# Kernel optimization log

Hardware: AMD Instinct MI355X
Metric: run time of the kernel (lower is better)

The kernel has to match this reference:

```python
import jax, jax.numpy as jnp
import numpy as np

# Rates 40MHz -> 60MHz => Fraction(1.5).limit_denominator(1000) = 3/2
UP, DOWN = 3, 2
MAX_RATE = max(UP, DOWN)
HALF_LEN = 10 * MAX_RATE                      # 30 (scipy.resample_poly default)
N_PRE_PAD = DOWN - (HALF_LEN % DOWN)          # 2
N_PRE_REMOVE = (HALF_LEN + N_PRE_PAD) // DOWN # 16
NUMTAPS_LS = 51
TAIL_ZEROS = 100
B, N = 8, 1048576


def _firwin_kaiser(numtaps, cutoff, beta):
    # scipy.signal.firwin(numtaps, cutoff, window=('kaiser', beta)), cutoff in Nyquist units
    m = np.arange(numtaps) - (numtaps - 1) / 2.0
    h = cutoff * np.sinc(cutoff * m)
    h *= np.kaiser(numtaps, beta)
    return h / h.sum()  # unit DC gain


def _band_int(k, f1, f2):
    # integral_{f1}^{f2} cos(pi*k*f) df, elementwise over integer array k
    k = np.asarray(k, dtype=float)
    safe = np.where(k == 0.0, 1.0, np.pi * k)
    return np.where(k == 0.0, f2 - f1, (np.sin(np.pi * k * f2) - np.sin(np.pi * k * f1)) / safe)


def _firls(numtaps, bands, desired):
    # Type-I linear-phase least-squares FIR (constant desired per band, unit weights)
    M = (numtaps - 1) // 2
    k = np.arange(M + 1)
    Q = np.zeros((M + 1, M + 1))
    rhs = np.zeros(M + 1)
    for f1, f2, d in zip(bands[0::2], bands[1::2], desired[0::2]):
        km = k[:, None] - k[None, :]
        kp = k[:, None] + k[None, :]
        Q += 0.5 * (_band_int(km, f1, f2) + _band_int(kp, f1, f2))
        rhs += d * _band_int(k, f1, f2)
    a = np.linalg.solve(Q, rhs)  # A(f) = sum_n a[n] cos(pi n f)
    half = a / 2.0
    half[0] = a[0]
    return np.concatenate([half[:0:-1], half])  # symmetric impulse response


def setup_inputs() -> dict:
    key = jax.random.key(0)
    x = jax.random.normal(key, (B, N), dtype=jnp.float32)
    # resample_poly anti-imaging filter, scaled by UP, with scipy's zero pre-padding
    h = _firwin_kaiser(2 * HALF_LEN + 1, 1.0 / MAX_RATE, 5.0) * UP
    h = np.concatenate([np.zeros(N_PRE_PAD), h])
    cutoff = DOWN / UP
    b = _firls(NUMTAPS_LS, [0.0, cutoff, cutoff + 0.1, 1.0], [1.0, 1.0, 0.0, 0.0])
    return {
        'x': x,
        'h_resample': jnp.asarray(h, jnp.float32),
        'b_fir': jnp.asarray(b, jnp.float32),
    }


def reference(x, h_resample, b_fir):
    b_sz, n = x.shape
    n_in = b_sz * n
    n_out = n_in * UP // DOWN + (1 if (n_in * UP) % DOWN else 0)
    xf = x.reshape(-1)
    Lh = h_resample.shape[0]
    # Fused polyphase resample: full convolution of UP-zero-stuffed signal
    # with h (flipped for true convolution), decimated by DOWN.
    y = jax.lax.conv_general_dilated(
        xf[None, None, :], h_resample[::-1][None, None, :],
        window_strides=(DOWN,), padding=[(Lh - 1, Lh - 1)],
        lhs_dilation=(UP,),
        dimension_numbers=('NCH', 'OIH', 'NCH'))[0, 0]
    u = y[N_PRE_REMOVE:N_PRE_REMOVE + n_out]               # == scipy.resample_poly
    up_padded = jnp.concatenate([u, jnp.zeros((TAIL_ZEROS,), x.dtype)])
    Lb = b_fir.shape[0]
    # lfilter(b, 1, .) == causal FIR: left-pad Lb-1 zeros, same-length output
    filt = jax.lax.conv_general_dilated(
        up_padded[None, None, :], b_fir[::-1][None, None, :],
        window_strides=(1,), padding=[(Lb - 1, 0)],
        dimension_numbers=('NCH', 'OIH', 'NCH'))[0, 0]
    total = n_out + TAIL_ZEROS
    per_b = total // b_sz
    return filt[:b_sz * per_b].reshape(b_sz, per_b)
```

## Files before the change

### kernel.cpp

```cpp
#include <hip/hip_runtime.h>


#define TPB 256
#define RPT 12
#define OTILE (TPB * RPT)
#define WREG 144
#define NTAPS 55
#define CPSTRIDE 56

#define SLOT(c) ((c) ^ (((c) >> 3) & 7))

__global__ __launch_bounds__(TPB) void prep_k(
    const float* __restrict__ x, const float* __restrict__ h,
    const float* __restrict__ b, float* __restrict__ cp,
    float* __restrict__ out, int n_in, int n_out, int out_size)
{
    __shared__ float h_s[63];
    __shared__ float b_s[51];
    __shared__ float x_s[64];
    __shared__ float u_s[50];

    const int tid = threadIdx.x;
    if (tid < 63) h_s[tid] = h[tid];
    if (tid < 51) b_s[tid] = b[tid];

    if (blockIdx.x == 0) {
        __syncthreads();
        for (int idx = tid; idx < 3 * CPSTRIDE; idx += TPB) {
            const int p = idx / CPSTRIDE;
            const int k = idx - p * CPSTRIDE;
            float acc = 0.0f;
            if (k < NTAPS) {
                const int j = p + 3 * k;
                for (int m = 0; m <= 50; ++m) {
                    const int hi = j - 2 * m;
                    if (hi >= 0 && hi <= 62) acc += b_s[m] * h_s[hi];
                }
            }
            cp[idx] = acc;
        }
    } else if (blockIdx.x == 1) {
        if (tid < 44) x_s[tid] = (tid < n_in) ? x[tid] : 0.0f;
        __syncthreads();
        if (tid < 50) {
            const int s  = 2 * tid + 32;
            const int p0 = s % 3;
            const int q  = s / 3;
            float u = 0.0f;
            #pragma unroll
            for (int i = 0; i <= 20; ++i) {
                const int xi = q - i;
                u += h_s[p0 + 3 * i] * ((xi >= 0) ? x_s[xi] : 0.0f);
            }
            u_s[tid] = u;
        }
        __syncthreads();
        if (tid < 50) {
            float acc = 0.0f;
            for (int t = 0; t <= tid; ++t) acc += b_s[tid - t] * u_s[t];
            out[tid] = acc;
        }
    } else {
        const int t0   = n_out - 50;
        const int qmin = (2 * t0 + 32) / 3;
        const int xb   = qmin - 20;
        if (tid < 64) {
            const int xi = xb + tid;
            x_s[tid] = (xi >= 0 && xi < n_in) ? x[xi] : 0.0f;
        }
        __syncthreads();
        if (tid < 50) {
            const int t  = t0 + tid;
            const int s  = 2 * t + 32;
            const int p0 = s % 3;
            const int q  = s / 3;
            const int base = q - xb;
            float u = 0.0f;
            #pragma unroll
            for (int i = 0; i <= 20; ++i)
                u += h_s[p0 + 3 * i] * x_s[base - i];
            u_s[tid] = u;
        }
        __syncthreads();
        const int n_tail = out_size - n_out;
        if (tid < n_tail) {
            float acc = 0.0f;
            for (int j = tid; j <= 49; ++j) acc += b_s[tid + 50 - j] * u_s[j];
            out[n_out + tid] = acc;
        }
    }
}

__device__ __forceinline__ float co(const int i, const int c0,
                                    const int c1, const int c2) {
    const int ln = i & 63;
    const int v = (i < 64)  ? __builtin_amdgcn_readlane(c0, ln)
                : (i < 128) ? __builtin_amdgcn_readlane(c1, ln)
                            : __builtin_amdgcn_readlane(c2, ln);
    return __int_as_float(v);
}

#define GRP12(g, A, B, C, D) {                                          \
    const float q2x = co(112 + 4*(g), cc0, cc1, cc2);                   \
    const float q2y = co(113 + 4*(g), cc0, cc1, cc2);                   \
    const float q2z = co(114 + 4*(g), cc0, cc1, cc2);                   \
    const float q2w = co(115 + 4*(g), cc0, cc1, cc2);                   \
    const float q1x = co( 56 + 4*(g), cc0, cc1, cc2);                   \
    const float q1y = co( 57 + 4*(g), cc0, cc1, cc2);                   \
    const float q1z = co( 58 + 4*(g), cc0, cc1, cc2);                   \
    const float q1w = co( 59 + 4*(g), cc0, cc1, cc2);                   \
    const float q0x = co(      4*(g), cc0, cc1, cc2);                   \
    const float q0y = co(  1 + 4*(g), cc0, cc1, cc2);                   \
    const float q0z = co(  2 + 4*(g), cc0, cc1, cc2);                   \
    const float q0w = co(  3 + 4*(g), cc0, cc1, cc2);                   \
                                                               \
    a0  += q2x * C.z;  a1  += q1x * C.w;  a2  += q0x * B.x;             \
    a3  += q2x * B.x;  a4  += q1x * B.y;  a5  += q0x * B.z;             \
    a6  += q2x * B.z;  a7  += q1x * B.w;  a8  += q0x * A.x;             \
    a9  += q2x * A.x;  a10 += q1x * A.y;  a11 += q0x * A.z;             \
                                                               \
    a0  += q2y * C.y;  a1  += q1y * C.z;  a2  += q0y * C.w;             \
    a3  += q2y * C.w;  a4  += q1y * B.x;  a5  += q0y * B.y;             \
    a6  += q2y * B.y;  a7  += q1y * B.z;  a8  += q0y * B.w;             \
    a9  += q2y * B.w;  a10 += q1y * A.x;  a11 += q0y * A.y;             \
                                                               \
    a0  += q2z * C.x;  a1  += q1z * C.y;  a2  += q0z * C.z;             \
    a3  += q2z * C.z;  a4  += q1z * C.w;  a5  += q0z * B.x;             \
    a6  += q2z * B.x;  a7  += q1z * B.y;  a8  += q0z * B.z;             \
    a9  += q2z * B.z;  a10 += q1z * B.w;  a11 += q0z * A.x;             \
                                                               \
    a0  += q2w * D.w;  a1  += q1w * C.x;  a2  += q0w * C.y;             \
    a3  += q2w * C.y;  a4  += q1w * C.z;  a5  += q0w * C.w;             \
    a6  += q2w * C.w;  a7  += q1w * B.x;  a8  += q0w * B.y;             \
    a9  += q2w * B.y;  a10 += q1w * B.z;  a11 += q0w * B.w; }

#define GRP12T(g, A, B, C) {                                            \
    const float q2x = co(112 + 4*(g), cc0, cc1, cc2);                   \
    const float q2y = co(113 + 4*(g), cc0, cc1, cc2);                   \
    const float q2z = co(114 + 4*(g), cc0, cc1, cc2);                   \
    const float q1x = co( 56 + 4*(g), cc0, cc1, cc2);                   \
    const float q1y = co( 57 + 4*(g), cc0, cc1, cc2);                   \
    const float q1z = co( 58 + 4*(g), cc0, cc1, cc2);                   \
    const float q0x = co(      4*(g), cc0, cc1, cc2);                   \
    const float q0y = co(  1 + 4*(g), cc0, cc1, cc2);                   \
    const float q0z = co(  2 + 4*(g), cc0, cc1, cc2);                   \
    a0  += q2x * C.z;  a1  += q1x * C.w;  a2  += q0x * B.x;             \
    a3  += q2x * B.x;  a4  += q1x * B.y;  a5  += q0x * B.z;             \
    a6  += q2x * B.z;  a7  += q1x * B.w;  a8  += q0x * A.x;             \
    a9  += q2x * A.x;  a10 += q1x * A.y;  a11 += q0x * A.z;             \
    a0  += q2y * C.y;  a1  += q1y * C.z;  a2  += q0y * C.w;             \
    a3  += q2y * C.w;  a4  += q1y * B.x;  a5  += q0y * B.y;             \
    a6  += q2y * B.y;  a7  += q1y * B.z;  a8  += q0y * B.w;             \
    a9  += q2y * B.w;  a10 += q1y * A.x;  a11 += q0y * A.y;             \
    a0  += q2z * C.x;  a1  += q1z * C.y;  a2  += q0z * C.z;             \
    a3  += q2z * C.z;  a4  += q1z * C.w;  a5  += q0z * B.x;             \
    a6  += q2z * B.x;  a7  += q1z * B.y;  a8  += q0z * B.z;             \
    a9  += q2z * B.z;  a10 += q1z * B.w;  a11 += q0z * A.x; }

__global__ __launch_bounds__(TPB) void fused_fast(
    const float* __restrict__ x, const float* __restrict__ cp,
    float* __restrict__ out, int n_in, int n_out)
{
    __shared__ float4 xs4[4 * WREG];

    const int tid = threadIdx.x;
    const int w   = tid >> 6;
    const int l   = tid & 63;
    const int bt  = blockIdx.x;
    const int o0  = bt * OTILE;
    const int n_tile0 = 2048 * bt - 44;
    const int wreg = w * WREG;

    const int cc0 = __float_as_int(cp[l]);
    const int cc1 = __float_as_int(cp[l + 64]);
    const int cc2 = __float_as_int(cp[(l < 40) ? (128 + l) : 128]);

    const bool interior = (n_tile0 >= 0) && (n_tile0 + 2104 <= n_in);
    if (interior) {
        const float4* gw = (const float4*)(x + n_tile0) + 128 * w;
        const float4 g0 = gw[l];
        const float4 g1 = gw[l + 64];
        xs4[wreg + SLOT(l)]      = g0;
        xs4[wreg + SLOT(l + 64)] = g1;
        if (l < 14) {
            xs4[wreg + SLOT(l + 128)] = gw[l + 128];
        }
    } else {
        const int fb0 = n_tile0 + 512 * w;
        #pragma unroll
        for (int s = 0; s < 3; ++s) {
            const int c = l + 64 * s;
            if (c > 141) break;
            const int fb = fb0 + 4 * c;
            float4 v;
            v.x = (fb + 0 >= 0 && fb + 0 < n_in) ? x[fb + 0] : 0.0f;
            v.y = (fb + 1 >= 0 && fb + 1 < n_in) ? x[fb + 1] : 0.0f;
            v.z = (fb + 2 >= 0 && fb + 2 < n_in) ? x[fb + 2] : 0.0f;
            v.w = (fb + 3 >= 0 && fb + 3 < n_in) ? x[fb + 3] : 0.0f;
            xs4[wreg + SLOT(c)] = v;
        }
    }

    float a0 = 0.f, a1 = 0.f, a2 = 0.f, a3  = 0.f, a4  = 0.f, a5  = 0.f;
    float a6 = 0.f, a7 = 0.f, a8 = 0.f, a9  = 0.f, a10 = 0.f, a11 = 0.f;

#define XS(j) xs4[wreg + SLOT(2 * l + (j))]
    {
        float4 r0 = XS(15), r1 = XS(14), r2 = XS(13),
               r3 = XS(12), r4 = XS(11), r5 = XS(10);
        GRP12( 0, r0, r1, r2, r3);  r0 = XS(9);
        GRP12( 1, r1, r2, r3, r4);  r1 = XS(8);
        GRP12( 2, r2, r3, r4, r5);  r2 = XS(7);
        GRP12( 3, r3, r4, r5, r0);  r3 = XS(6);
        GRP12( 4, r4, r5, r0, r1);  r4 = XS(5);
        GRP12( 5, r5, r0, r1, r2);  r5 = XS(4);
        GRP12( 6, r0, r1, r2, r3);  r0 = XS(3);
        GRP12( 7, r1, r2, r3, r4);  r1 = XS(2);
        GRP12( 8, r2, r3, r4, r5);  r2 = XS(1);
        GRP12( 9, r3, r4, r5, r0);  r3 = XS(0);
        GRP12(10, r4, r5, r0, r1);
        GRP12(11, r5, r0, r1, r2);
        GRP12(12, r0, r1, r2, r3);
        GRP12T(13, r1, r2, r3);
    }
#undef XS

    const int ob = o0 + RPT * tid;
    if (ob >= 50 && ob + 11 < n_out) {
        float4* o4 = (float4*)(out + ob);
        o4[0] = make_float4(a0, a1, a2,  a3);
        o4[1] = make_float4(a4, a5, a6,  a7);
        o4[2] = make_float4(a8, a9, a10, a11);
    } else {
        const float accs[RPT] = {a0, a1, a2, a3, a4, a5, a6, a7, a8, a9, a10, a11};
#pragma unroll
        for (int d = 0; d < RPT; ++d) {
            const int o = ob + d;
            if (o >= 50 && o < n_out) out[o] = accs[d];
        }
    }
}

extern "C" void kernel_launch(void* const* d_in, const int* in_sizes, int n_in_arrs,
                              void* d_out, int out_size, void* d_ws, size_t ws_size,
                              hipStream_t stream) {
    const float* x = (const float*)d_in[0];
    const float* h = (const float*)d_in[1];
    const float* b = (const float*)d_in[2];
    float* out = (float*)d_out;
    float* cp  = (float*)d_ws;

    const int n_in  = in_sizes[0];
    const int n_out = (int)((long long)n_in * 3 / 2);

    prep_k<<<3, TPB, 0, stream>>>(x, h, b, cp, out, n_in, n_out, out_size);

    const int nblocks = (n_out + OTILE - 1) / OTILE;
    fused_fast<<<nblocks, TPB, 0, stream>>>(x, cp, out, n_in, n_out);
}
```

Measured before the change: 106.6 us.

## Process two output tiles per block with both input loads issued upfront

Each block now computes two consecutive output tiles instead of one, so the grid is half as large. Global loads for both tiles' input windows go into registers before the first tile's compute starts, with a sched_barrier keeping the loads grouped. The second tile's load latency is meant to hide behind the first tile's FMA work. The cost is extra live registers for the second tile's staged data and fewer blocks available to hide latency through occupancy.

```diff
diff --git a/kernel.cpp b/kernel.cpp
--- a/kernel.cpp
+++ b/kernel.cpp
@@ -157,6 +157,59 @@
     a6  += q2z * B.x;  a7  += q1z * B.y;  a8  += q0z * B.z;             \
     a9  += q2z * B.z;  a10 += q1z * B.w;  a11 += q0z * A.x; }
 
+#define EDGE_STAGE(NT) {                                                \
+    const int fb0 = (NT) + 512 * w;                                     \
+    _Pragma("unroll")                                                   \
+    for (int s = 0; s < 3; ++s) {                                       \
+        const int c = l + 64 * s;                                       \
+        if (c > 141) break;                                             \
+        const int fb = fb0 + 4 * c;                                     \
+        float4 v;                                                       \
+        v.x = (fb + 0 >= 0 && fb + 0 < n_in) ? x[fb + 0] : 0.0f;        \
+        v.y = (fb + 1 >= 0 && fb + 1 < n_in) ? x[fb + 1] : 0.0f;        \
+        v.z = (fb + 2 >= 0 && fb + 2 < n_in) ? x[fb + 2] : 0.0f;        \
+        v.w = (fb + 3 >= 0 && fb + 3 < n_in) ? x[fb + 3] : 0.0f;        \
+        xs4[wreg + SLOT(c)] = v;                                        \
+    } }
+
+#define XS(j) xs4[wreg + SLOT(2 * l + (j))]
+
+#define TILE_COMPUTE(OB) {                                              \
+    float a0 = 0.f, a1 = 0.f, a2 = 0.f, a3  = 0.f, a4  = 0.f, a5 = 0.f;\
+    float a6 = 0.f, a7 = 0.f, a8 = 0.f, a9  = 0.f, a10 = 0.f, a11 = 0.f;\
+    {                                                                   \
+        float4 r0 = XS(15), r1 = XS(14), r2 = XS(13),                   \
+               r3 = XS(12), r4 = XS(11), r5 = XS(10);                   \
+        GRP12( 0, r0, r1, r2, r3);  r0 = XS(9);                         \
+        GRP12( 1, r1, r2, r3, r4);  r1 = XS(8);                         \
+        GRP12( 2, r2, r3, r4, r5);  r2 = XS(7);                         \
+        GRP12( 3, r3, r4, r5, r0);  r3 = XS(6);                         \
+        GRP12( 4, r4, r5, r0, r1);  r4 = XS(5);                         \
+        GRP12( 5, r5, r0, r1, r2);  r5 = XS(4);                         \
+        GRP12( 6, r0, r1, r2, r3);  r0 = XS(3);                         \
+        GRP12( 7, r1, r2, r3, r4);  r1 = XS(2);                         \
+        GRP12( 8, r2, r3, r4, r5);  r2 = XS(1);                         \
+        GRP12( 9, r3, r4, r5, r0);  r3 = XS(0);                         \
+        GRP12(10, r4, r5, r0, r1);                                      \
+        GRP12(11, r5, r0, r1, r2);                                      \
+        GRP12(12, r0, r1, r2, r3);                                      \
+        GRP12T(13, r1, r2, r3);                                         \
+    }                                                                   \
+    const int ob_ = (OB);                                               \
+    if (ob_ >= 50 && ob_ + 11 < n_out) {                                \
+        float4* o4 = (float4*)(out + ob_);             \
+        o4[0] = make_float4(a0, a1, a2,  a3);                           \
+        o4[1] = make_float4(a4, a5, a6,  a7);                           \
+        o4[2] = make_float4(a8, a9, a10, a11);                          \
+    } else {                                                            \
+        const float accs[RPT] = {a0,a1,a2,a3,a4,a5,a6,a7,a8,a9,a10,a11};\
+        _Pragma("unroll")                                               \
+        for (int d = 0; d < RPT; ++d) {                                 \
+            const int o = ob_ + d;                                      \
+            if (o >= 50 && o < n_out) out[o] = accs[d];                 \
+        }                                                               \
+    } }
+
 __global__ __launch_bounds__(TPB) void fused_fast(
     const float* __restrict__ x, const float* __restrict__ cp,
     float* __restrict__ out, int n_in, int n_out)
@@ -167,78 +220,50 @@
     const int w   = tid >> 6;
     const int l   = tid & 63;
     const int bt  = blockIdx.x;
-    const int o0  = bt * OTILE;
-    const int n_tile0 = 2048 * bt - 44;
+    const int o0  = bt * (2 * OTILE);
+    const int ntA = 4096 * bt - 44;
+    const int ntB = ntA + 2048;
     const int wreg = w * WREG;
 
     const int cc0 = __float_as_int(cp[l]);
     const int cc1 = __float_as_int(cp[l + 64]);
     const int cc2 = __float_as_int(cp[(l < 40) ? (128 + l) : 128]);
 
-    const bool interior = (n_tile0 >= 0) && (n_tile0 + 2104 <= n_in);
-    if (interior) {
-        const float4* gw = (const float4*)(x + n_tile0) + 128 * w;
-        const float4 g0 = gw[l];
-        const float4 g1 = gw[l + 64];
-        xs4[wreg + SLOT(l)]      = g0;
-        xs4[wreg + SLOT(l + 64)] = g1;
-        if (l < 14) {
-            xs4[wreg + SLOT(l + 128)] = gw[l + 128];
-        }
+    const bool intA = (ntA >= 0) && (ntA + 2104 <= n_in);
+    const bool intB = (ntB >= 0) && (ntB + 2104 <= n_in);
+
+    float4 ga0, ga1, ga2, gb0, gb1, gb2;
+    if (intA) {
+        const float4* gw = (const float4*)(x + ntA) + 128 * w;
+        ga0 = gw[l];
+        ga1 = gw[l + 64];
+        if (l < 14) ga2 = gw[l + 128];
+    }
+    if (intB) {
+        const float4* gw = (const float4*)(x + ntB) + 128 * w;
+        gb0 = gw[l];
+        gb1 = gw[l + 64];
+        if (l < 14) gb2 = gw[l + 128];
+    }
+    __builtin_amdgcn_sched_barrier(0);
+
+    if (intA) {
+        xs4[wreg + SLOT(l)]      = ga0;
+        xs4[wreg + SLOT(l + 64)] = ga1;
+        if (l < 14) xs4[wreg + SLOT(l + 128)] = ga2;
     } else {
-        const int fb0 = n_tile0 + 512 * w;
-        #pragma unroll
-        for (int s = 0; s < 3; ++s) {
-            const int c = l + 64 * s;
-            if (c > 141) break;
-            const int fb = fb0 + 4 * c;
-            float4 v;
-            v.x = (fb + 0 >= 0 && fb + 0 < n_in) ? x[fb + 0] : 0.0f;
-            v.y = (fb + 1 >= 0 && fb + 1 < n_in) ? x[fb + 1] : 0.0f;
-            v.z = (fb + 2 >= 0 && fb + 2 < n_in) ? x[fb + 2] : 0.0f;
-            v.w = (fb + 3 >= 0 && fb + 3 < n_in) ? x[fb + 3] : 0.0f;
-            xs4[wreg + SLOT(c)] = v;
-        }
-    }
-
-    float a0 = 0.f, a1 = 0.f, a2 = 0.f, a3  = 0.f, a4  = 0.f, a5  = 0.f;
-    float a6 = 0.f, a7 = 0.f, a8 = 0.f, a9  = 0.f, a10 = 0.f, a11 = 0.f;
-
-#define XS(j) xs4[wreg + SLOT(2 * l + (j))]
-    {
-        float4 r0 = XS(15), r1 = XS(14), r2 = XS(13),
-               r3 = XS(12), r4 = XS(11), r5 = XS(10);
-        GRP12( 0, r0, r1, r2, r3);  r0 = XS(9);
-        GRP12( 1, r1, r2, r3, r4);  r1 = XS(8);
-        GRP12( 2, r2, r3, r4, r5);  r2 = XS(7);
-        GRP12( 3, r3, r4, r5, r0);  r3 = XS(6);
-        GRP12( 4, r4, r5, r0, r1);  r4 = XS(5);
-        GRP12( 5, r5, r0, r1, r2);  r5 = XS(4);
-        GRP12( 6, r0, r1, r2, r3);  r0 = XS(3);
-        GRP12( 7, r1, r2, r3, r4);  r1 = XS(2);
-        GRP12( 8, r2, r3, r4, r5);  r2 = XS(1);
-        GRP12( 9, r3, r4, r5, r0);  r3 = XS(0);
-        GRP12(10, r4, r5, r0, r1);
-        GRP12(11, r5, r0, r1, r2);
-        GRP12(12, r0, r1, r2, r3);
-        GRP12T(13, r1, r2, r3);
-    }
-#undef XS
-
-    const int ob = o0 + RPT * tid;
-    if (ob >= 50 && ob + 11 < n_out) {
-        float4* o4 = (float4*)(out + ob);
-        o4[0] = make_float4(a0, a1, a2,  a3);
-        o4[1] = make_float4(a4, a5, a6,  a7);
-        o4[2] = make_float4(a8, a9, a10, a11);
+        EDGE_STAGE(ntA);
+    }
+    TILE_COMPUTE(o0 + RPT * tid);
+
+    if (intB) {
+        xs4[wreg + SLOT(l)]      = gb0;
+        xs4[wreg + SLOT(l + 64)] = gb1;
+        if (l < 14) xs4[wreg + SLOT(l + 128)] = gb2;
     } else {
-        const float accs[RPT] = {a0, a1, a2, a3, a4, a5, a6, a7, a8, a9, a10, a11};
-#pragma unroll
-        for (int d = 0; d < RPT; ++d) {
-            const int o = ob + d;
-            if (o >= 50 && o < n_out) out[o] = accs[d];
-        }
-    }
+        EDGE_STAGE(ntB);
+    }
+    TILE_COMPUTE(o0 + OTILE + RPT * tid);
 }
 
 extern "C" void kernel_launch(void* const* d_in, const int* in_sizes, int n_in_arrs,
@@ -255,6 +280,6 @@
 
     prep_k<<<3, TPB, 0, stream>>>(x, h, b, cp, out, n_in, n_out, out_size);
 
-    const int nblocks = (n_out + OTILE - 1) / OTILE;
+    const int nblocks = (n_out + 2 * OTILE - 1) / (2 * OTILE);
     fused_fast<<<nblocks, TPB, 0, stream>>>(x, cp, out, n_in, n_out);
 }
```

New measurement: 108.0 us. About the same (+1.3%).
